# Optimization experiments

Hardware: AMD Instinct MI355X
Metric: run time of the kernel (lower is better)

## Reference

```python
import jax, jax.numpy as jnp
import numpy as np

N_NODES = 50000
N_EDGES = 800000
IN_DIM, HID_DIM, OUT_DIM = 128, 128, 64


def setup_inputs() -> dict:
    key = jax.random.key(0)
    ks = jax.random.split(key, 10)
    s = lambda d: 1.0 / np.sqrt(d)
    return {
        "feat": jax.random.normal(ks[0], (N_NODES, IN_DIM), jnp.float32),
        "W_self1": jax.random.normal(ks[1], (IN_DIM, HID_DIM), jnp.float32) * s(IN_DIM),
        "W_neigh1": jax.random.normal(ks[2], (IN_DIM, HID_DIM), jnp.float32) * s(IN_DIM),
        "b1": jnp.zeros((HID_DIM,), jnp.float32),
        "W_self2": jax.random.normal(ks[3], (HID_DIM, OUT_DIM), jnp.float32) * s(HID_DIM),
        "W_neigh2": jax.random.normal(ks[4], (HID_DIM, OUT_DIM), jnp.float32) * s(HID_DIM),
        "b2": jnp.zeros((OUT_DIM,), jnp.float32),
        "src": jax.random.randint(ks[5], (N_EDGES,), 0, N_NODES),
        "dst": jax.random.randint(ks[6], (N_EDGES,), 0, N_NODES),
        "neg_src": jax.random.randint(ks[7], (N_EDGES,), 0, N_NODES),
        "neg_dst": jax.random.randint(ks[8], (N_EDGES,), 0, N_NODES),
    }


def sage_conv(feat, src, dst, W_self, W_neigh, b):
    # DGL SAGEConv('mean'): out = feat @ W_self + mean_{u->v}(feat_u) @ W_neigh + b
    msg = feat[src]                                                      # [E, D] gather
    agg = jax.ops.segment_sum(msg, dst, num_segments=N_NODES)            # [N, D]
    deg = jax.ops.segment_sum(jnp.ones((src.shape[0], 1), feat.dtype), dst,
                              num_segments=N_NODES)                      # [N, 1]
    h_neigh = agg / jnp.maximum(deg, 1.0)                                # zero for isolated nodes
    return feat @ W_self + h_neigh @ W_neigh + b


def edge_dot(feat, src, dst):
    # dgl.function.u_dot_v -> [E, 1]
    return jnp.sum(feat[src] * feat[dst], axis=-1, keepdims=True)


def reference(feat, W_self1, W_neigh1, b1, W_self2, W_neigh2, b2,
              src, dst, neg_src, neg_dst):
    h = jax.nn.relu(sage_conv(feat, src, dst, W_self1, W_neigh1, b1))
    h = sage_conv(h, src, dst, W_self2, W_neigh2, b2)
    return (edge_dot(h, src, dst), edge_dot(h, neg_src, neg_dst))
```

## Files before the change

### kernel.cpp

```cpp
#include <hip/hip_runtime.h>

#define IN_DIM 128
#define HID_DIM 128
#define OUT_DIM 64

typedef short bf16x8 __attribute__((ext_vector_type(8)));
typedef float f32x4  __attribute__((ext_vector_type(4)));

__device__ inline float bflo(unsigned int u) { return __uint_as_float(u << 16); }
__device__ inline float bfhi(unsigned int u) { return __uint_as_float(u & 0xffff0000u); }
__device__ inline unsigned short f2bf(float f) {
    unsigned int b = __float_as_uint(f);
    return (unsigned short)((b + 0x7FFFu + ((b >> 16) & 1u)) >> 16);
}
__device__ inline unsigned int pack2(float a, float b) {
    return (unsigned int)f2bf(a) | ((unsigned int)f2bf(b) << 16);
}
__device__ inline float dot8(uint4 a, uint4 b) {
    return bflo(a.x) * bflo(b.x) + bfhi(a.x) * bfhi(b.x)
         + bflo(a.y) * bflo(b.y) + bfhi(a.y) * bfhi(b.y)
         + bflo(a.z) * bflo(b.z) + bfhi(a.z) * bfhi(b.z)
         + bflo(a.w) * bflo(b.w) + bfhi(a.w) * bfhi(b.w);
}

__global__ void zero_cnt_kernel(uint4* __restrict__ p, int n4) {
    int i = blockIdx.x * blockDim.x + threadIdx.x;
    if (i < n4) p[i] = (uint4){0, 0, 0, 0};
}

__global__ void wtrans_hist_kernel(const float* __restrict__ Ws1, const float* __restrict__ Wn1,
                                   const float* __restrict__ Ws2, const float* __restrict__ Wn2,
                                   unsigned short* __restrict__ Wt1, unsigned short* __restrict__ Wt2,
                                   const int* __restrict__ dst, int* __restrict__ cnt,
                                   unsigned short* __restrict__ rank, int E) {
    if ((int)blockIdx.x < 24) {
        int tid = (int)blockIdx.x * 256 + threadIdx.x;
        if (tid < 4096) {
            int c = tid >> 4, k0 = (tid & 15) << 3;
            const float* W = (c < 128) ? (Ws1 + c) : (Wn1 + (c - 128));
            ushort4 a, b;
            a.x = f2bf(W[(size_t)(k0 + 0) * 128]); a.y = f2bf(W[(size_t)(k0 + 1) * 128]);
            a.z = f2bf(W[(size_t)(k0 + 2) * 128]); a.w = f2bf(W[(size_t)(k0 + 3) * 128]);
            b.x = f2bf(W[(size_t)(k0 + 4) * 128]); b.y = f2bf(W[(size_t)(k0 + 5) * 128]);
            b.z = f2bf(W[(size_t)(k0 + 6) * 128]); b.w = f2bf(W[(size_t)(k0 + 7) * 128]);
            *(ushort4*)&Wt1[c * 128 + k0]     = a;
            *(ushort4*)&Wt1[c * 128 + k0 + 4] = b;
        } else if (tid < 6144) {
            int t = tid - 4096;
            int c = t >> 4, k0 = (t & 15) << 3;
            const float* W = (c < 64) ? (Ws2 + c) : (Wn2 + (c - 64));
            ushort4 a, b;
            a.x = f2bf(W[(size_t)(k0 + 0) * 64]); a.y = f2bf(W[(size_t)(k0 + 1) * 64]);
            a.z = f2bf(W[(size_t)(k0 + 2) * 64]); a.w = f2bf(W[(size_t)(k0 + 3) * 64]);
            b.x = f2bf(W[(size_t)(k0 + 4) * 64]); b.y = f2bf(W[(size_t)(k0 + 5) * 64]);
            b.z = f2bf(W[(size_t)(k0 + 6) * 64]); b.w = f2bf(W[(size_t)(k0 + 7) * 64]);
            *(ushort4*)&Wt2[c * 128 + k0]     = a;
            *(ushort4*)&Wt2[c * 128 + k0 + 4] = b;
        }
        return;
    }
    int e = ((int)blockIdx.x - 24) * 256 + threadIdx.x;
    if (e < E) rank[e] = (unsigned short)atomicAdd(&cnt[dst[e]], 1);
}

__global__ void block_sums_kernel(const int* __restrict__ cnt, int* __restrict__ partial, int N) {
    __shared__ int s[256];
    int i = blockIdx.x * 256 + threadIdx.x;
    s[threadIdx.x] = (i < N) ? cnt[i] : 0;
    __syncthreads();
    for (int o = 128; o > 0; o >>= 1) {
        if (threadIdx.x < o) s[threadIdx.x] += s[threadIdx.x + o];
        __syncthreads();
    }
    if (threadIdx.x == 0) partial[blockIdx.x] = s[0];
}

__global__ void scan_chunks_kernel(const int* __restrict__ cnt, const int* __restrict__ partial,
                                   int* __restrict__ row_ptr, int N, int NB) {
    __shared__ int s[256];
    const int t = threadIdx.x;
    s[t] = (t < NB && t < (int)blockIdx.x) ? partial[t] : 0;
    __syncthreads();
    for (int o = 128; o > 0; o >>= 1) {
        if (t < o) s[t] += s[t + o];
        __syncthreads();
    }
    const int base = s[0];
    __syncthreads();
    int i = blockIdx.x * 256 + t;
    int v = (i < N) ? cnt[i] : 0;
    s[t] = v;
    __syncthreads();
    for (int o = 1; o < 256; o <<= 1) {
        int tv = (t >= o) ? s[t - o] : 0;
        __syncthreads();
        s[t] += tv;
        __syncthreads();
    }
    int incl = s[t];
    if (i < N) row_ptr[i] = base + incl - v;
    if (i == N - 1) row_ptr[N] = base + incl;
}

__global__ __launch_bounds__(256) void gemm1_fill_kernel(
        const float* __restrict__ x,
        const unsigned short* __restrict__ Wt,
        const float* __restrict__ bias,
        unsigned short* __restrict__ hsb,
        unsigned short* __restrict__ t,
        int N, int FB,
        const int* __restrict__ src,
        const int* __restrict__ dst,
        const int* __restrict__ row_ptr,
        const unsigned short* __restrict__ rank,
        unsigned short* __restrict__ col_src,
        int E) {
    constexpr int DOUT = HID_DIM;
    constexpr int K   = 128;
    constexpr int MT  = 64;
    constexpr int SL  = 2 * DOUT / 4;
    constexpr int TN  = SL / 16;
    constexpr int TM  = MT / 16;
    constexpr int KS  = K / 32;
    constexpr int LDA = K + 8;

    __shared__ unsigned short sA[MT][LDA];

    const int tid = threadIdx.x;

    if ((int)blockIdx.x < FB) {
        int base = (int)blockIdx.x * 1024;
        #pragma unroll
        for (int k = 0; k < 4; ++k) {
            int e = base + k * 256 + tid;
            if (e < E) {
                int d = dst[e];
                col_src[row_ptr[d] + (int)rank[e]] = (unsigned short)src[e];
            }
        }
        return;
    }

    const int w   = tid >> 6;
    const int l   = tid & 63;
    const int l16 = l & 15;
    const int lhi = l >> 4;
    const int n0  = ((int)blockIdx.x - FB) * MT;

    #pragma unroll
    for (int it = 0; it < 8; ++it) {
        int flat = it * 256 + tid;
        int r  = flat >> 5;
        int c4 = flat & 31;
        float4 v = {0, 0, 0, 0};
        if (n0 + r < N) v = *(const float4*)&x[(size_t)(n0 + r) * K + c4 * 4];
        ushort4 p;
        p.x = f2bf(v.x); p.y = f2bf(v.y); p.z = f2bf(v.z); p.w = f2bf(v.w);
        *(ushort4*)&sA[r][c4 * 4] = p;
    }

    bf16x8 breg[TN][KS];
    float  bval[TN];
    #pragma unroll
    for (int tn = 0; tn < TN; ++tn) {
        const int c = w * SL + tn * 16 + l16;
        bval[tn] = (c < DOUT) ? bias[c] : 0.0f;
        #pragma unroll
        for (int ks = 0; ks < KS; ++ks)
            breg[tn][ks] = *(const bf16x8*)&Wt[c * 128 + ks * 32 + lhi * 8];
    }
    __syncthreads();

    f32x4 acc[TN][TM];
    #pragma unroll
    for (int tn = 0; tn < TN; ++tn)
        #pragma unroll
        for (int tm = 0; tm < TM; ++tm)
            acc[tn][tm] = (f32x4){0.0f, 0.0f, 0.0f, 0.0f};

    #pragma unroll
    for (int ks = 0; ks < KS; ++ks) {
        bf16x8 a[TM];
        #pragma unroll
        for (int tm = 0; tm < TM; ++tm)
            a[tm] = *(const bf16x8*)&sA[tm * 16 + l16][ks * 32 + lhi * 8];
        #pragma unroll
        for (int tn = 0; tn < TN; ++tn)
            #pragma unroll
            for (int tm = 0; tm < TM; ++tm)
                acc[tn][tm] = __builtin_amdgcn_mfma_f32_16x16x32_bf16(
                    a[tm], breg[tn][ks], acc[tn][tm], 0, 0, 0);
    }

    #pragma unroll
    for (int tn = 0; tn < TN; ++tn) {
        const int c = w * SL + tn * 16 + l16;
        const bool self = (c < DOUT);
        const int cc = self ? c : c - DOUT;
        #pragma unroll
        for (int tm = 0; tm < TM; ++tm) {
            #pragma unroll
            for (int r = 0; r < 4; ++r) {
                const int n = n0 + tm * 16 + lhi * 4 + r;
                if (n < N) {
                    const unsigned short v = f2bf(acc[tn][tm][r] + bval[tn]);
                    if (self) hsb[(size_t)n * DOUT + cc] = v;
                    else      t  [(size_t)n * DOUT + cc] = v;
                }
            }
        }
    }
}

__global__ void gather_mean128_kernel(const unsigned short* __restrict__ t,
                                      const unsigned short* __restrict__ base,
                                      const int* __restrict__ row_ptr,
                                      const unsigned short* __restrict__ col_src,
                                      unsigned short* __restrict__ out, int N) {
    int node = (blockIdx.x * blockDim.x + threadIdx.x) >> 6;
    int lane = threadIdx.x & 63;
    if (node >= N) return;
    const int beg = row_ptr[node], end = row_ptr[node + 1];
    const float rdeg = 1.0f / fmaxf((float)(end - beg), 1.0f);
    const int off = lane * 2;

    float a0x = 0, a0y = 0, a1x = 0, a1y = 0, a2x = 0, a2y = 0, a3x = 0, a3y = 0;
    int i = beg;
    for (; i + 4 <= end; i += 4) {
        int s0 = col_src[i], s1 = col_src[i + 1], s2 = col_src[i + 2], s3 = col_src[i + 3];
        unsigned int u0 = *(const unsigned int*)&t[(size_t)s0 * 128 + off];
        unsigned int u1 = *(const unsigned int*)&t[(size_t)s1 * 128 + off];
        unsigned int u2 = *(const unsigned int*)&t[(size_t)s2 * 128 + off];
        unsigned int u3 = *(const unsigned int*)&t[(size_t)s3 * 128 + off];
        a0x += bflo(u0); a0y += bfhi(u0);
        a1x += bflo(u1); a1y += bfhi(u1);
        a2x += bflo(u2); a2y += bfhi(u2);
        a3x += bflo(u3); a3y += bfhi(u3);
    }
    for (; i < end; ++i) {
        unsigned int u = *(const unsigned int*)&t[(size_t)col_src[i] * 128 + off];
        a0x += bflo(u); a0y += bfhi(u);
    }
    float ax = (a0x + a1x) + (a2x + a3x);
    float ay = (a0y + a1y) + (a2y + a3y);
    unsigned int ub = *(const unsigned int*)&base[(size_t)node * 128 + off];
    float ox = fmaxf(bflo(ub) + ax * rdeg, 0.0f);
    float oy = fmaxf(bfhi(ub) + ay * rdeg, 0.0f);
    *(unsigned int*)&out[(size_t)node * 128 + off] = pack2(ox, oy);
}

__global__ __launch_bounds__(256) void gemm2_kernel(
        const unsigned short* __restrict__ x,
        const unsigned short* __restrict__ Wt,
        const float* __restrict__ bias,
        unsigned short* __restrict__ hsb2,
        unsigned short* __restrict__ t2,
        int N) {
    constexpr int DOUT = OUT_DIM;
    constexpr int K   = 128;
    constexpr int MT  = 64;
    constexpr int SL  = 2 * DOUT / 4;
    constexpr int TN  = SL / 16;
    constexpr int TM  = MT / 16;
    constexpr int KS  = K / 32;
    constexpr int LDA = K + 8;

    __shared__ unsigned short sA[MT][LDA];

    const int tid = threadIdx.x;
    const int w   = tid >> 6;
    const int l   = tid & 63;
    const int l16 = l & 15;
    const int lhi = l >> 4;
    const int n0  = (int)blockIdx.x * MT;

    #pragma unroll
    for (int it = 0; it < 4; ++it) {
        int flat = it * 256 + tid;
        int r  = flat >> 4;
        int c8 = flat & 15;
        uint4 v = {0, 0, 0, 0};
        if (n0 + r < N) v = *(const uint4*)&x[(size_t)(n0 + r) * K + c8 * 8];
        *(uint4*)&sA[r][c8 * 8] = v;
    }

    bf16x8 breg[TN][KS];
    float  bval[TN];
    #pragma unroll
    for (int tn = 0; tn < TN; ++tn) {
        const int c = w * SL + tn * 16 + l16;
        bval[tn] = (c < DOUT) ? bias[c] : 0.0f;
        #pragma unroll
        for (int ks = 0; ks < KS; ++ks)
            breg[tn][ks] = *(const bf16x8*)&Wt[c * 128 + ks * 32 + lhi * 8];
    }
    __syncthreads();

    f32x4 acc[TN][TM];
    #pragma unroll
    for (int tn = 0; tn < TN; ++tn)
        #pragma unroll
        for (int tm = 0; tm < TM; ++tm)
            acc[tn][tm] = (f32x4){0.0f, 0.0f, 0.0f, 0.0f};

    #pragma unroll
    for (int ks = 0; ks < KS; ++ks) {
        bf16x8 a[TM];
        #pragma unroll
        for (int tm = 0; tm < TM; ++tm)
            a[tm] = *(const bf16x8*)&sA[tm * 16 + l16][ks * 32 + lhi * 8];
        #pragma unroll
        for (int tn = 0; tn < TN; ++tn)
            #pragma unroll
            for (int tm = 0; tm < TM; ++tm)
                acc[tn][tm] = __builtin_amdgcn_mfma_f32_16x16x32_bf16(
                    a[tm], breg[tn][ks], acc[tn][tm], 0, 0, 0);
    }

    #pragma unroll
    for (int tn = 0; tn < TN; ++tn) {
        const int c = w * SL + tn * 16 + l16;
        const bool self = (c < DOUT);
        const int cc = self ? c : c - DOUT;
        #pragma unroll
        for (int tm = 0; tm < TM; ++tm) {
            #pragma unroll
            for (int r = 0; r < 4; ++r) {
                const int n = n0 + tm * 16 + lhi * 4 + r;
                if (n < N) {
                    const unsigned short v = f2bf(acc[tn][tm][r] + bval[tn]);
                    if (self) hsb2[(size_t)n * DOUT + cc] = v;
                    else      t2  [(size_t)n * DOUT + cc] = v;
                }
            }
        }
    }
}

__global__ void gather_mean64_kernel(const unsigned short* __restrict__ t,
                                     const unsigned short* __restrict__ base,
                                     const int* __restrict__ row_ptr,
                                     const unsigned short* __restrict__ col_src,
                                     unsigned short* __restrict__ out, int N) {
    int tid  = blockIdx.x * blockDim.x + threadIdx.x;
    int node = (tid >> 6) * 2 + ((tid >> 5) & 1);
    int m    = tid & 31;
    if (node >= N) return;
    const int beg = row_ptr[node], end = row_ptr[node + 1];
    const float rdeg = 1.0f / fmaxf((float)(end - beg), 1.0f);
    const int off = m * 2;

    float a0x = 0, a0y = 0, a1x = 0, a1y = 0, a2x = 0, a2y = 0, a3x = 0, a3y = 0;
    int i = beg;
    for (; i + 4 <= end; i += 4) {
        int s0 = col_src[i], s1 = col_src[i + 1], s2 = col_src[i + 2], s3 = col_src[i + 3];
        unsigned int u0 = *(const unsigned int*)&t[(size_t)s0 * 64 + off];
        unsigned int u1 = *(const unsigned int*)&t[(size_t)s1 * 64 + off];
        unsigned int u2 = *(const unsigned int*)&t[(size_t)s2 * 64 + off];
        unsigned int u3 = *(const unsigned int*)&t[(size_t)s3 * 64 + off];
        a0x += bflo(u0); a0y += bfhi(u0);
        a1x += bflo(u1); a1y += bfhi(u1);
        a2x += bflo(u2); a2y += bfhi(u2);
        a3x += bflo(u3); a3y += bfhi(u3);
    }
    for (; i < end; ++i) {
        unsigned int u = *(const unsigned int*)&t[(size_t)col_src[i] * 64 + off];
        a0x += bflo(u); a0y += bfhi(u);
    }
    float ax = (a0x + a1x) + (a2x + a3x);
    float ay = (a0y + a1y) + (a2y + a3y);
    unsigned int ub = *(const unsigned int*)&base[(size_t)node * 64 + off];
    *(unsigned int*)&out[(size_t)node * 64 + off] =
        pack2(bflo(ub) + ax * rdeg, bfhi(ub) + ay * rdeg);
}

__global__ void edge_dot_kernel(const unsigned short* __restrict__ h,
                                const int* __restrict__ src,
                                const int* __restrict__ dst,
                                const int* __restrict__ nsrc,
                                const int* __restrict__ ndst,
                                float* __restrict__ out,
                                int E) {
    int tid = blockIdx.x * blockDim.x + threadIdx.x;
    int eg = tid >> 2;
    int l  = tid & 3;
    if (eg >= 2 * E) return;
    int s, t;
    if (eg < E) { s = src[eg];      t = dst[eg]; }
    else        { s = nsrc[eg - E]; t = ndst[eg - E]; }
    const uint4* pa = (const uint4*)&h[(size_t)s * OUT_DIM + l * 16];
    const uint4* pb = (const uint4*)&h[(size_t)t * OUT_DIM + l * 16];
    uint4 a0 = pa[0], a1 = pa[1];
    uint4 b0 = pb[0], b1 = pb[1];
    float v = dot8(a0, b0) + dot8(a1, b1);
    v += __shfl_xor(v, 2, 4);
    v += __shfl_xor(v, 1, 4);
    if (l == 0) out[eg] = v;
}

extern "C" void kernel_launch(void* const* d_in, const int* in_sizes, int n_in,
                              void* d_out, int out_size, void* d_ws, size_t ws_size,
                              hipStream_t stream) {
    const float* feat = (const float*)d_in[0];
    const float* Ws1  = (const float*)d_in[1];
    const float* Wn1  = (const float*)d_in[2];
    const float* b1   = (const float*)d_in[3];
    const float* Ws2  = (const float*)d_in[4];
    const float* Wn2  = (const float*)d_in[5];
    const float* b2   = (const float*)d_in[6];
    const int* src  = (const int*)d_in[7];
    const int* dst  = (const int*)d_in[8];
    const int* nsrc = (const int*)d_in[9];
    const int* ndst = (const int*)d_in[10];
    const int E = in_sizes[7];
    const int N = in_sizes[0] / IN_DIM;
    const int NB = (N + 255) / 256;
    const int NT = (N + 63) / 64;
    const int FB = (E + 1023) / 1024;
    const int HB = (E + 255) / 256;

    char* wsb = (char*)d_ws;
    unsigned short* Wt1  = (unsigned short*)wsb;
    unsigned short* Wt2  = Wt1 + 256 * 128;
    unsigned short* t1   = Wt2 + 128 * 128;
    unsigned short* hs1b = t1 + (size_t)N * HID_DIM;
    unsigned short* h1   = hs1b + (size_t)N * HID_DIM;
    unsigned short* t2   = h1 + (size_t)N * HID_DIM;
    unsigned short* hs2b = t2 + (size_t)N * OUT_DIM;
    unsigned short* h2   = hs2b + (size_t)N * OUT_DIM;
    int* cnt             = (int*)(h2 + (size_t)N * OUT_DIM);
    int* row_ptr         = cnt + N;
    int* partial         = row_ptr + N + 1;
    unsigned short* rank    = (unsigned short*)(partial + 256);
    unsigned short* col_src = rank + E;

    {
        int n4 = (N + 3) / 4;
        zero_cnt_kernel<<<(n4 + 255) / 256, 256, 0, stream>>>((uint4*)cnt, n4);
    }

    wtrans_hist_kernel<<<24 + HB, 256, 0, stream>>>(
        Ws1, Wn1, Ws2, Wn2, Wt1, Wt2, dst, cnt, rank, E);
    block_sums_kernel<<<NB, 256, 0, stream>>>(cnt, partial, N);
    scan_chunks_kernel<<<NB, 256, 0, stream>>>(cnt, partial, row_ptr, N, NB);

    gemm1_fill_kernel<<<FB + NT, 256, 0, stream>>>(
        feat, Wt1, b1, hs1b, t1, N, FB,
        src, dst, row_ptr, rank, col_src, E);

    gather_mean128_kernel<<<(N * 64 + 255) / 256, 256, 0, stream>>>(
        t1, hs1b, row_ptr, col_src, h1, N);

    gemm2_kernel<<<NT, 256, 0, stream>>>(
        h1, Wt2, b2, hs2b, t2, N);

    {
        int waves = (N + 1) / 2;
        gather_mean64_kernel<<<(waves * 64 + 255) / 256, 256, 0, stream>>>(
            t2, hs2b, row_ptr, col_src, h2, N);
    }

    {
        int total = 2 * E * 4;
        edge_dot_kernel<<<(total + 255) / 256, 256, 0, stream>>>(
            h2, src, dst, nsrc, ndst, (float*)d_out, E);
    }
}
```

Before: 182.4 us.

## Halve gemm1 row tile and process two edges per thread group in edge_dot

The first GEMM kernel's row tile shrinks from 64 to 32 rows, so twice as many smaller blocks are launched and spread across the CUs. Separately, edge_dot now has each 4-lane group compute two consecutive edges. This gives each thread more independent gathers in flight and lets results be written as float2. The trade-off is more GEMM blocks that each reload the weights, and higher register use in edge_dot.

```diff
diff --git a/kernel.cpp b/kernel.cpp
--- a/kernel.cpp
+++ b/kernel.cpp
@@ -117,7 +117,7 @@
         int E) {
     constexpr int DOUT = HID_DIM;
     constexpr int K   = 128;
-    constexpr int MT  = 64;
+    constexpr int MT  = 32;
     constexpr int SL  = 2 * DOUT / 4;
     constexpr int TN  = SL / 16;
     constexpr int TM  = MT / 16;
@@ -148,7 +148,7 @@
     const int n0  = ((int)blockIdx.x - FB) * MT;
 
     #pragma unroll
-    for (int it = 0; it < 8; ++it) {
+    for (int it = 0; it < 4; ++it) {
         int flat = it * 256 + tid;
         int r  = flat >> 5;
         int c4 = flat & 31;
@@ -382,20 +382,45 @@
                                 float* __restrict__ out,
                                 int E) {
     int tid = blockIdx.x * blockDim.x + threadIdx.x;
-    int eg = tid >> 2;
-    int l  = tid & 3;
-    if (eg >= 2 * E) return;
-    int s, t;
-    if (eg < E) { s = src[eg];      t = dst[eg]; }
-    else        { s = nsrc[eg - E]; t = ndst[eg - E]; }
-    const uint4* pa = (const uint4*)&h[(size_t)s * OUT_DIM + l * 16];
-    const uint4* pb = (const uint4*)&h[(size_t)t * OUT_DIM + l * 16];
-    uint4 a0 = pa[0], a1 = pa[1];
-    uint4 b0 = pb[0], b1 = pb[1];
-    float v = dot8(a0, b0) + dot8(a1, b1);
-    v += __shfl_xor(v, 2, 4);
-    v += __shfl_xor(v, 1, 4);
-    if (l == 0) out[eg] = v;
+    int g = tid >> 2;
+    int l = tid & 3;
+    int e0 = g * 2;
+    if (e0 >= 2 * E) return;
+    int e1 = e0 + 1;
+    const bool has1 = (e1 < 2 * E);
+
+    int s0, t0;
+    if (e0 < E) { s0 = src[e0];      t0 = dst[e0]; }
+    else        { s0 = nsrc[e0 - E]; t0 = ndst[e0 - E]; }
+    int s1 = s0, t1 = t0;
+    if (has1) {
+        if (e1 < E) { s1 = src[e1];      t1 = dst[e1]; }
+        else        { s1 = nsrc[e1 - E]; t1 = ndst[e1 - E]; }
+    }
+
+    const uint4* pa0 = (const uint4*)&h[(size_t)s0 * OUT_DIM + l * 16];
+    const uint4* pb0 = (const uint4*)&h[(size_t)t0 * OUT_DIM + l * 16];
+    const uint4* pa1 = (const uint4*)&h[(size_t)s1 * OUT_DIM + l * 16];
+    const uint4* pb1 = (const uint4*)&h[(size_t)t1 * OUT_DIM + l * 16];
+    uint4 a00 = pa0[0], a01 = pa0[1];
+    uint4 b00 = pb0[0], b01 = pb0[1];
+    uint4 a10 = pa1[0], a11 = pa1[1];
+    uint4 b10 = pb1[0], b11 = pb1[1];
+
+    float v0 = dot8(a00, b00) + dot8(a01, b01);
+    float v1 = dot8(a10, b10) + dot8(a11, b11);
+    v0 += __shfl_xor(v0, 2, 4);
+    v0 += __shfl_xor(v0, 1, 4);
+    v1 += __shfl_xor(v1, 2, 4);
+    v1 += __shfl_xor(v1, 1, 4);
+    if (l == 0) {
+        if (has1) {
+            float2 o = {v0, v1};
+            *(float2*)&out[e0] = o;
+        } else {
+            out[e0] = v0;
+        }
+    }
 }
 
 extern "C" void kernel_launch(void* const* d_in, const int* in_sizes, int n_in,
@@ -415,7 +440,8 @@
     const int E = in_sizes[7];
     const int N = in_sizes[0] / IN_DIM;
     const int NB = (N + 255) / 256;
-    const int NT = (N + 63) / 64;
+    const int NT1 = (N + 31) / 32;
+    const int NT2 = (N + 63) / 64;
     const int FB = (E + 1023) / 1024;
     const int HB = (E + 255) / 256;
 
@@ -444,14 +470,14 @@
     block_sums_kernel<<<NB, 256, 0, stream>>>(cnt, partial, N);
     scan_chunks_kernel<<<NB, 256, 0, stream>>>(cnt, partial, row_ptr, N, NB);
 
-    gemm1_fill_kernel<<<FB + NT, 256, 0, stream>>>(
+    gemm1_fill_kernel<<<FB + NT1, 256, 0, stream>>>(
         feat, Wt1, b1, hs1b, t1, N, FB,
         src, dst, row_ptr, rank, col_src, E);
 
     gather_mean128_kernel<<<(N * 64 + 255) / 256, 256, 0, stream>>>(
         t1, hs1b, row_ptr, col_src, h1, N);
 
-    gemm2_kernel<<<NT, 256, 0, stream>>>(
+    gemm2_kernel<<<NT2, 256, 0, stream>>>(
         h1, Wt2, b2, hs2b, t2, N);
 
     {
@@ -461,7 +487,8 @@
     }
 
     {
-        int total = 2 * E * 4;
+        int groups = (2 * E + 1) / 2;
+        int total = groups * 4;
         edge_dot_kernel<<<(total + 255) / 256, 256, 0, stream>>>(
             h2, src, dst, nsrc, ndst, (float*)d_out, E);
     }
```

Result: no change. 184.5 us (+1.1%).
